# Performance work log

Measured on AMD Instinct MI355X. Metric: run time of the kernel, lower is better.

Reference implementation:

```python
import jax, jax.numpy as jnp
import numpy as np

D_MODEL = 1024
NHEAD = 16
HEAD_DIM = D_MODEL // NHEAD
NPOS_MAX = 1000
SEQ = 1024
BATCH = 4


def setup_inputs() -> dict:
    key = jax.random.key(0)
    ks = jax.random.split(key, 10)
    s = 0.02
    return {
        "x": jax.random.normal(ks[0], (SEQ, BATCH, D_MODEL), dtype=jnp.float32),
        "Wq": jax.random.normal(ks[1], (D_MODEL, D_MODEL), dtype=jnp.float32) * s,
        "bq": jnp.zeros((D_MODEL,), dtype=jnp.float32),
        "Wk": jax.random.normal(ks[2], (D_MODEL, D_MODEL), dtype=jnp.float32) * s,
        "bk": jnp.zeros((D_MODEL,), dtype=jnp.float32),
        "Wv": jax.random.normal(ks[3], (D_MODEL, D_MODEL), dtype=jnp.float32) * s,
        "bv": jnp.zeros((D_MODEL,), dtype=jnp.float32),
        "Wo": jax.random.normal(ks[4], (D_MODEL, D_MODEL), dtype=jnp.float32) * s,
        "bo": jnp.zeros((D_MODEL,), dtype=jnp.float32),
        "pos_emb": jax.random.normal(ks[5], (1, HEAD_DIM, NPOS_MAX), dtype=jnp.float32) * s,
    }


def _cope(query, attn_logits, pos_emb):
    # query: (H,B,S,D); attn_logits: (H,B,S,S); pos_emb: (1,D,npos)
    gates = jax.nn.sigmoid(attn_logits)
    # reverse cumulative sum along the key axis
    pos = jnp.cumsum(gates[..., ::-1], axis=-1)[..., ::-1]
    pos = jnp.minimum(pos, NPOS_MAX - 1)
    pos_ceil = jnp.ceil(pos).astype(jnp.int32)
    pos_floor = jnp.floor(pos).astype(jnp.int32)
    # (H,B,S,npos): interpolation logits for every integer position
    logits_int = jnp.einsum("hbsd,dn->hbsn", query, pos_emb[0])
    logits_ceil = jnp.take_along_axis(logits_int, pos_ceil, axis=-1)
    logits_floor = jnp.take_along_axis(logits_int, pos_floor, axis=-1)
    w = pos - pos_floor.astype(pos.dtype)
    return logits_ceil * w + logits_floor * (1.0 - w)


def reference(x, Wq, bq, Wk, bk, Wv, bv, Wo, bo, pos_emb):
    S, B, _ = x.shape
    # torch Linear: x @ W.T + b; weights here are already (in,out) so x @ W + b
    def split_heads(t):
        # (S,B,d_model) -> (H,B,S,D)  (matches .view(S,B,H,D).transpose(0,2))
        return t.reshape(S, B, NHEAD, HEAD_DIM).transpose(2, 1, 0, 3)

    q = split_heads(x @ Wq + bq)
    k = split_heads(x @ Wk + bk)
    v = split_heads(x @ Wv + bv)

    scale = 1.0 / (HEAD_DIM ** 0.5)
    attn_logits = jnp.einsum("hbsd,hbtd->hbst", q, k) * scale
    attn_logits = attn_logits + _cope(q, attn_logits, pos_emb)
    attn = jax.nn.softmax(attn_logits, axis=-1)
    out = jnp.einsum("hbst,hbtd->hbsd", attn, v)
    # (H,B,S,D) -> (S,B,d_model)
    out = out.transpose(2, 1, 0, 3).reshape(S, B, D_MODEL)
    return out @ Wo + bo
```

## Files before the change

### kernel.cpp

```cpp
#include <hip/hip_runtime.h>
#include <hip/hip_bf16.h>

#define D_MODEL 1024
#define NHEAD 16
#define HEAD_DIM 64
#define SEQ 1024
#define BATCH 4

typedef unsigned short us;
typedef __attribute__((ext_vector_type(8))) short short8;
typedef __attribute__((ext_vector_type(4))) float f32x4;

#define MFMA16 __builtin_amdgcn_mfma_f32_16x16x32_bf16

__device__ __forceinline__ float sigmoidf_(float x) {
  return 1.0f / (1.0f + __expf(-x));
}
__device__ __forceinline__ us f2bf(float x) {
  union { float f; unsigned u; } v; v.f = x;
  unsigned r = v.u + 0x7fffu + ((v.u >> 16) & 1u);
  return (us)(r >> 16);
}
__device__ __forceinline__ float bf2f(us s) {
  union { unsigned u; float f; } v; v.u = ((unsigned)s) << 16; return v.f;
}
__device__ __forceinline__ void split_bf(float v, us& h, us& l) {
  h = f2bf(v);
  l = f2bf(v - bf2f(h));
}
__device__ __forceinline__ void async16(us* lds, const us* g) {
  __builtin_amdgcn_global_load_lds(
      (const __attribute__((address_space(1))) unsigned int*)(const void*)g,
      (__attribute__((address_space(3))) unsigned int*)(void*)lds, 16, 0, 0);
}

__global__ __launch_bounds__(256) void prep_k(
    const float* __restrict__ x, const float* __restrict__ Wq,
    const float* __restrict__ Wk, const float* __restrict__ Wv,
    const float* __restrict__ Wo, const float* __restrict__ pe,
    us* __restrict__ xh, us* __restrict__ xl, us* __restrict__ wqk,
    us* __restrict__ wvh, us* __restrict__ wvl, us* __restrict__ woh,
    us* __restrict__ wol, us* __restrict__ pet)
{
  __shared__ float tile[32][33];
  const int bid = blockIdx.x, tid = threadIdx.x;
  if (bid < 2048) {
    int i0 = bid * 2048 + tid * 8;
    float4 v0 = *(const float4*)(x + i0);
    float4 v1 = *(const float4*)(x + i0 + 4);
    float vv[8] = {v0.x, v0.y, v0.z, v0.w, v1.x, v1.y, v1.z, v1.w};
    short8 hh, ll;
    #pragma unroll
    for (int j = 0; j < 8; ++j) {
      us h, l; split_bf(vv[j], h, l);
      hh[j] = (short)h; ll[j] = (short)l;
    }
    *(short8*)(xh + i0) = hh;
    *(short8*)(xl + i0) = ll;
  } else if (bid < 6144) {
    int wj = bid - 2048;
    int w = wj >> 10, t = wj & 1023;
    int k0 = (t >> 5) * 32, n0 = (t & 31) * 32;
    const float* W = (w == 0) ? Wq : (w == 1) ? Wk : (w == 2) ? Wv : Wo;
    int tx = tid & 31, ty = tid >> 5;
    #pragma unroll
    for (int rep = 0; rep < 4; ++rep) {
      int ky = ty * 4 + rep;
      tile[ky][tx] = W[(size_t)(k0 + ky) * 1024 + n0 + tx];
    }
    __syncthreads();
    #pragma unroll
    for (int rep = 0; rep < 4; ++rep) {
      int ny = ty * 4 + rep;
      float v = tile[tx][ny];
      int n = n0 + ny, k = k0 + tx;
      if (w < 2) {
        wqk[(size_t)(w * 1024 + n) * 1024 + k] = f2bf(v);
      } else {
        us h, l; split_bf(v, h, l);
        us* dh = (w == 2) ? wvh : woh;
        us* dl = (w == 2) ? wvl : wol;
        dh[(size_t)n * 1024 + k] = h;
        dl[(size_t)n * 1024 + k] = l;
      }
    }
  } else {
    int pj = bid - 6144;
    int k0 = (pj & 1) * 32, n0 = (pj >> 1) * 32;
    int tx = tid & 31, ty = tid >> 5;
    #pragma unroll
    for (int rep = 0; rep < 4; ++rep) {
      int ky = ty * 4 + rep;
      tile[ky][tx] = (n0 + tx < 1000) ? pe[(size_t)(k0 + ky) * 1000 + n0 + tx] : 0.f;
    }
    __syncthreads();
    #pragma unroll
    for (int rep = 0; rep < 4; ++rep) {
      int ny = ty * 4 + rep;
      int n = n0 + ny;
      if (n < 1000) pet[(size_t)n * 64 + k0 + tx] = f2bf(tile[tx][ny]);
    }
  }
}

template<int TERMS, int TN>
__global__ __launch_bounds__(256) void mgemm(
    const us* __restrict__ A0, const us* __restrict__ A1,
    const us* __restrict__ B0, const us* __restrict__ B1,
    const float* __restrict__ bias0, const float* __restrict__ bias1,
    void* out0, void* out1, int mode)
{
  constexpr int PA = (TERMS == 3) ? 2 : 1;
  constexpr int NJ = TN / 32;
  constexpr int NW = TN / 2;
  __shared__ us As[PA][128][32];
  __shared__ us Bs[PA][TN][32];
  const int tid = threadIdx.x, ln = tid & 63, wv = tid >> 6;
  const int col = ln & 15, quad = ln >> 4;
  const int wr = wv >> 1, wc = wv & 1;
  const int m0 = blockIdx.y * 128, n0 = blockIdx.x * TN;
  const us* Ap[2] = {A0, A1};
  const us* Bp[2] = {B0, B1};

  f32x4 acc[4][NJ];
  #pragma unroll
  for (int i = 0; i < 4; ++i)
    #pragma unroll
    for (int j = 0; j < NJ; ++j) acc[i][j] = (f32x4){0.f, 0.f, 0.f, 0.f};

  for (int kt = 0; kt < 1024; kt += 32) {
    #pragma unroll
    for (int p = 0; p < PA; ++p)
      #pragma unroll
      for (int j = 0; j < 2; ++j) {
        int c = j * 256 + wv * 64 + ln;
        int m = c >> 2;
        int kq = (c & 3) ^ ((c >> 3) & 3);
        async16((us*)&As[p][0][0] + (size_t)(j * 256 + wv * 64) * 8,
                Ap[p] + (size_t)(m0 + m) * 1024 + kt + kq * 8);
      }
    #pragma unroll
    for (int p = 0; p < PA; ++p)
      #pragma unroll
      for (int j = 0; j < TN / 64; ++j) {
        int c = j * 256 + wv * 64 + ln;
        int n = c >> 2;
        int kq = (c & 3) ^ ((c >> 3) & 3);
        async16((us*)&Bs[p][0][0] + (size_t)(j * 256 + wv * 64) * 8,
                Bp[p] + (size_t)(n0 + n) * 1024 + kt + kq * 8);
      }
    __syncthreads();

    short8 a0[4], a1[4], b0[NJ], b1[NJ];
    #pragma unroll
    for (int i = 0; i < 4; ++i) {
      int r = wr * 64 + i * 16 + col;
      int q = quad ^ ((r >> 1) & 3);
      a0[i] = *(const short8*)&As[0][r][q * 8];
      if constexpr (TERMS == 3) a1[i] = *(const short8*)&As[1][r][q * 8];
    }
    #pragma unroll
    for (int j = 0; j < NJ; ++j) {
      int r = wc * NW + j * 16 + col;
      int q = quad ^ ((r >> 1) & 3);
      b0[j] = *(const short8*)&Bs[0][r][q * 8];
      if constexpr (TERMS == 3) b1[j] = *(const short8*)&Bs[1][r][q * 8];
    }
    #pragma unroll
    for (int i = 0; i < 4; ++i)
      #pragma unroll
      for (int j = 0; j < NJ; ++j) {
        acc[i][j] = MFMA16(a0[i], b0[j], acc[i][j], 0, 0, 0);
        if constexpr (TERMS == 3) {
          acc[i][j] = MFMA16(a0[i], b1[j], acc[i][j], 0, 0, 0);
          acc[i][j] = MFMA16(a1[i], b0[j], acc[i][j], 0, 0, 0);
        }
      }
    __syncthreads();
  }

  #pragma unroll
  for (int i = 0; i < 4; ++i)
    #pragma unroll
    for (int j = 0; j < NJ; ++j)
      #pragma unroll
      for (int r = 0; r < 4; ++r) {
        int grow = m0 + wr * 64 + i * 16 + quad * 4 + r;
        int gcol = n0 + wc * NW + j * 16 + col;
        float val = acc[i][j][r];
        if (mode == 0) {
          val += (gcol < 1024 ? bias0 : bias1)[gcol & 1023];
          int h = (gcol >> 6) & 15, d = gcol & 63, b = grow & 3, s = grow >> 2;
          ((us*)(gcol < 1024 ? out0 : out1))
              [(size_t)((h * 4 + b) * 1024 + s) * 64 + d] = f2bf(val);
        } else if (mode == 1) {
          val += bias0[gcol];
          int h = gcol >> 6, d = gcol & 63, b = grow & 3, s = grow >> 2;
          size_t idx = (size_t)((h * 4 + b) * 64 + d) * 1024 + s;
          us hh, ll; split_bf(val, hh, ll);
          ((us*)out0)[idx] = hh;
          ((us*)out1)[idx] = ll;
        } else {
          val += bias0[gcol];
          ((float*)out0)[(size_t)grow * 1024 + gcol] = val;
        }
      }
}

__global__ __launch_bounds__(1024) void attn_k(
    const us* __restrict__ qb, const us* __restrict__ kb,
    const us* __restrict__ vth, const us* __restrict__ vtl,
    const us* __restrict__ pet, us* __restrict__ ah, us* __restrict__ al)
{
  __shared__ us S_s[16][1032];
  __shared__ alignas(16) us li_s[16][1024];
  __shared__ float qinv_s[16];

  const int tid = threadIdx.x;
  const int lane = tid & 63;
  const int wv = tid >> 6;
  const int col = lane & 15;
  const int quad = lane >> 4;
  const int hb = blockIdx.y;
  const int s0 = blockIdx.x * 16;

  const us* Q = qb + ((size_t)hb * SEQ + s0) * HEAD_DIM;
  const us* K = kb + (size_t)hb * SEQ * HEAD_DIM;
  const us* Vh = vth + (size_t)hb * HEAD_DIM * SEQ;
  const us* Vl = vtl + (size_t)hb * HEAD_DIM * SEQ;

  short8 aq0 = *(const short8*)(Q + col * 64 + quad * 8);
  short8 aq1 = *(const short8*)(Q + col * 64 + 32 + quad * 8);

  #pragma unroll
  for (int kt = 0; kt < 4; ++kt) {
    int t0 = wv * 64 + kt * 16;
    const us* Kr = K + (size_t)(t0 + col) * 64;
    short8 b0 = *(const short8*)(Kr + quad * 8);
    short8 b1 = *(const short8*)(Kr + 32 + quad * 8);
    f32x4 sc = {0.f, 0.f, 0.f, 0.f};
    sc = MFMA16(aq0, b0, sc, 0, 0, 0);
    sc = MFMA16(aq1, b1, sc, 0, 0, 0);
    #pragma unroll
    for (int r = 0; r < 4; ++r)
      S_s[quad * 4 + r][t0 + col] = f2bf(sc[r] * 0.125f);
  }

  #pragma unroll
  for (int nt = 0; nt < 4; ++nt) {
    int n = wv * 64 + nt * 16 + col;
    int nn = (n < 1000) ? n : 999;
    short8 b0 = *(const short8*)(pet + (size_t)nn * 64 + quad * 8);
    short8 b1 = *(const short8*)(pet + (size_t)nn * 64 + 32 + quad * 8);
    f32x4 li = {0.f, 0.f, 0.f, 0.f};
    li = MFMA16(aq0, b0, li, 0, 0, 0);
    li = MFMA16(aq1, b1, li, 0, 0, 0);
    #pragma unroll
    for (int r = 0; r < 4; ++r)
      li_s[quad * 4 + r][n] = f2bf(li[r]);
  }
  __syncthreads();

  {
    const int q = wv;
    const us* Sp = &S_s[q][lane * 16];
    float s[16], suf[16];
    #pragma unroll
    for (int j = 0; j < 16; ++j) s[j] = bf2f(Sp[j]);
    float run = 0.f;
    #pragma unroll
    for (int j = 15; j >= 0; --j) {
      run += sigmoidf_(s[j]);
      suf[j] = run;
    }
    float v = run;
    #pragma unroll
    for (int off = 1; off < 64; off <<= 1) {
      float u = __shfl_down(v, off);
      v += (lane + off < 64) ? u : 0.f;
    }
    float after = v - run;
    float lg[16];
    float m = -1e30f;
    #pragma unroll
    for (int j = 0; j < 16; ++j) {
      float p = fminf(after + suf[j], 999.0f);
      float fl = floorf(p);
      int fi = (int)fl;
      int ci = (int)ceilf(p);
      float w = p - fl;
      float lf = bf2f(li_s[q][fi]);
      float lc = bf2f(li_s[q][ci]);
      lg[j] = s[j] + lc * w + lf * (1.f - w);
      m = fmaxf(m, lg[j]);
    }
    #pragma unroll
    for (int off = 1; off < 64; off <<= 1) m = fmaxf(m, __shfl_xor(m, off));
    float rs = 0.f;
    us* Pp = &S_s[q][lane * 16];
    #pragma unroll
    for (int j = 0; j < 16; ++j) {
      float e = __expf(lg[j] - m);
      rs += e;
      Pp[j] = f2bf(e);
    }
    #pragma unroll
    for (int off = 1; off < 64; off <<= 1) rs += __shfl_xor(rs, off);
    if (lane == 0) qinv_s[q] = 1.0f / rs;
  }
  __syncthreads();

  const int wk = wv >> 2, wd = wv & 3;
  const int d0 = wd * 16;
  f32x4 o = {0.f, 0.f, 0.f, 0.f};
  #pragma unroll
  for (int kt = 0; kt < 8; ++kt) {
    int t0 = wk * 256 + kt * 32;
    short8 a = *(const short8*)&S_s[col][t0 + quad * 8];
    short8 bh = *(const short8*)(Vh + (size_t)(d0 + col) * 1024 + t0 + quad * 8);
    short8 bl = *(const short8*)(Vl + (size_t)(d0 + col) * 1024 + t0 + quad * 8);
    o = MFMA16(a, bh, o, 0, 0, 0);
    o = MFMA16(a, bl, o, 0, 0, 0);
  }
  __syncthreads();
  f32x4* red = (f32x4*)&li_s[0][0];
  red[wv * 64 + lane] = o;
  __syncthreads();
  if (wv < 4) {
    f32x4 t0v = red[(0 * 4 + wv) * 64 + lane];
    f32x4 t1v = red[(1 * 4 + wv) * 64 + lane];
    f32x4 t2v = red[(2 * 4 + wv) * 64 + lane];
    f32x4 t3v = red[(3 * 4 + wv) * 64 + lane];
    const int b_ = hb & 3, h = hb >> 2;
    #pragma unroll
    for (int r = 0; r < 4; ++r) {
      int q = quad * 4 + r;
      float val = (t0v[r] + t1v[r] + t2v[r] + t3v[r]) * qinv_s[q];
      size_t idx = (size_t)((s0 + q) * 4 + b_) * 1024 + h * 64 + wv * 16 + col;
      us hh, ll; split_bf(val, hh, ll);
      ah[idx] = hh;
      al[idx] = ll;
    }
  }
}

extern "C" void kernel_launch(void* const* d_in, const int* in_sizes, int n_in,
                              void* d_out, int out_size, void* d_ws, size_t ws_size,
                              hipStream_t stream) {
  const float* x  = (const float*)d_in[0];
  const float* Wq = (const float*)d_in[1];
  const float* bq = (const float*)d_in[2];
  const float* Wk = (const float*)d_in[3];
  const float* bk = (const float*)d_in[4];
  const float* Wv = (const float*)d_in[5];
  const float* bv = (const float*)d_in[6];
  const float* Wo = (const float*)d_in[7];
  const float* bo = (const float*)d_in[8];
  const float* pe = (const float*)d_in[9];

  us* w = (us*)d_ws;
  us* xh  = w;
  us* xl  = w + 4194304;
  us* wqk = w + 8388608;
  us* wvh = w + 10485760;
  us* wvl = w + 11534336;
  us* woh = w + 12582912;
  us* wol = w + 13631488;
  us* pet = w + 14680064;
  us* qb  = w + 14745600;
  us* kb  = w + 18939904;
  us* vth = w + 23134208;
  us* vtl = w + 27328512;
  us* ah  = w + 31522816;
  us* al  = w + 35717120;

  prep_k<<<6208, 256, 0, stream>>>(x, Wq, Wk, Wv, Wo, pe,
                                   xh, xl, wqk, wvh, wvl, woh, wol, pet);
  mgemm<1, 128><<<dim3(16, 32), 256, 0, stream>>>(
      xh, nullptr, wqk, nullptr, bq, bk, qb, kb, 0);
  mgemm<3, 64><<<dim3(16, 32), 256, 0, stream>>>(
      xh, xl, wvh, wvl, bv, bv, vth, vtl, 1);
  attn_k<<<dim3(64, 64), 1024, 0, stream>>>(qb, kb, vth, vtl, pet, ah, al);
  mgemm<3, 64><<<dim3(16, 32), 256, 0, stream>>>(
      ah, al, woh, wol, bo, bo, (void*)d_out, nullptr, 2);
}
```

Baseline: 473.3 us.

## Drop V low-part split, remap attention block order, vectorize LDS score access

The V projection now stores only a single bf16 value instead of a hi/lo split pair, so the P·V product in the attention kernel issues one MFMA and one global load per step instead of two. The attention grid is flattened into a 1D index that interleaves head/batch pairs across consecutive blocks, which changes cache locality for K/V reads. Score reads and probability writes in shared memory now use 16-byte vector accesses. The lower V precision cuts memory traffic and matrix work but may increase numerical error against the fp32 reference.

Result: faster. 403.8 us (-14.7%).

```diff
diff --git a/kernel.cpp b/kernel.cpp
--- a/kernel.cpp
+++ b/kernel.cpp
@@ -197,9 +197,7 @@
           val += bias0[gcol];
           int h = gcol >> 6, d = gcol & 63, b = grow & 3, s = grow >> 2;
           size_t idx = (size_t)((h * 4 + b) * 64 + d) * 1024 + s;
-          us hh, ll; split_bf(val, hh, ll);
-          ((us*)out0)[idx] = hh;
-          ((us*)out1)[idx] = ll;
+          ((us*)out0)[idx] = f2bf(val);
         } else {
           val += bias0[gcol];
           ((float*)out0)[(size_t)grow * 1024 + gcol] = val;
@@ -209,8 +207,8 @@
 
 __global__ __launch_bounds__(1024) void attn_k(
     const us* __restrict__ qb, const us* __restrict__ kb,
-    const us* __restrict__ vth, const us* __restrict__ vtl,
-    const us* __restrict__ pet, us* __restrict__ ah, us* __restrict__ al)
+    const us* __restrict__ vth, const us* __restrict__ pet,
+    us* __restrict__ ah, us* __restrict__ al)
 {
   __shared__ us S_s[16][1032];
   __shared__ alignas(16) us li_s[16][1024];
@@ -221,13 +219,13 @@
   const int wv = tid >> 6;
   const int col = lane & 15;
   const int quad = lane >> 4;
-  const int hb = blockIdx.y;
-  const int s0 = blockIdx.x * 16;
+  const int id = blockIdx.x;
+  const int hb = ((id >> 3) & 7) * 8 + (id & 7);
+  const int s0 = (id >> 6) * 16;
 
   const us* Q = qb + ((size_t)hb * SEQ + s0) * HEAD_DIM;
   const us* K = kb + (size_t)hb * SEQ * HEAD_DIM;
   const us* Vh = vth + (size_t)hb * HEAD_DIM * SEQ;
-  const us* Vl = vtl + (size_t)hb * HEAD_DIM * SEQ;
 
   short8 aq0 = *(const short8*)(Q + col * 64 + quad * 8);
   short8 aq1 = *(const short8*)(Q + col * 64 + 32 + quad * 8);
@@ -263,10 +261,13 @@
 
   {
     const int q = wv;
-    const us* Sp = &S_s[q][lane * 16];
+    short8 s8a = *(const short8*)&S_s[q][lane * 16];
+    short8 s8b = *(const short8*)&S_s[q][lane * 16 + 8];
     float s[16], suf[16];
     #pragma unroll
-    for (int j = 0; j < 16; ++j) s[j] = bf2f(Sp[j]);
+    for (int j = 0; j < 8; ++j) s[j] = bf2f((us)s8a[j]);
+    #pragma unroll
+    for (int j = 0; j < 8; ++j) s[8 + j] = bf2f((us)s8b[j]);
     float run = 0.f;
     #pragma unroll
     for (int j = 15; j >= 0; --j) {
@@ -297,15 +298,23 @@
     #pragma unroll
     for (int off = 1; off < 64; off <<= 1) m = fmaxf(m, __shfl_xor(m, off));
     float rs = 0.f;
-    us* Pp = &S_s[q][lane * 16];
-    #pragma unroll
-    for (int j = 0; j < 16; ++j) {
+    short8 p8a, p8b;
+    #pragma unroll
+    for (int j = 0; j < 8; ++j) {
       float e = __expf(lg[j] - m);
       rs += e;
-      Pp[j] = f2bf(e);
+      p8a[j] = (short)f2bf(e);
+    }
+    #pragma unroll
+    for (int j = 0; j < 8; ++j) {
+      float e = __expf(lg[8 + j] - m);
+      rs += e;
+      p8b[j] = (short)f2bf(e);
     }
     #pragma unroll
     for (int off = 1; off < 64; off <<= 1) rs += __shfl_xor(rs, off);
+    *(short8*)&S_s[q][lane * 16] = p8a;
+    *(short8*)&S_s[q][lane * 16 + 8] = p8b;
     if (lane == 0) qinv_s[q] = 1.0f / rs;
   }
   __syncthreads();
@@ -318,9 +327,7 @@
     int t0 = wk * 256 + kt * 32;
     short8 a = *(const short8*)&S_s[col][t0 + quad * 8];
     short8 bh = *(const short8*)(Vh + (size_t)(d0 + col) * 1024 + t0 + quad * 8);
-    short8 bl = *(const short8*)(Vl + (size_t)(d0 + col) * 1024 + t0 + quad * 8);
     o = MFMA16(a, bh, o, 0, 0, 0);
-    o = MFMA16(a, bl, o, 0, 0, 0);
   }
   __syncthreads();
   f32x4* red = (f32x4*)&li_s[0][0];
@@ -370,7 +377,6 @@
   us* qb  = w + 14745600;
   us* kb  = w + 18939904;
   us* vth = w + 23134208;
-  us* vtl = w + 27328512;
   us* ah  = w + 31522816;
   us* al  = w + 35717120;
 
@@ -379,8 +385,8 @@
   mgemm<1, 128><<<dim3(16, 32), 256, 0, stream>>>(
       xh, nullptr, wqk, nullptr, bq, bk, qb, kb, 0);
   mgemm<3, 64><<<dim3(16, 32), 256, 0, stream>>>(
-      xh, xl, wvh, wvl, bv, bv, vth, vtl, 1);
-  attn_k<<<dim3(64, 64), 1024, 0, stream>>>(qb, kb, vth, vtl, pet, ah, al);
+      xh, xl, wvh, wvl, bv, bv, vth, nullptr, 1);
+  attn_k<<<dim3(4096), 1024, 0, stream>>>(qb, kb, vth, pet, ah, al);
   mgemm<3, 64><<<dim3(16, 32), 256, 0, stream>>>(
       ah, al, woh, wol, bo, bo, (void*)d_out, nullptr, 2);
 }
```
